# Optimization experiments

Measured on AMD Instinct MI355X. Metric: run time of the kernel, lower is better.

Reference implementation:

```python
import math
import jax, jax.numpy as jnp
import numpy as np

B, N, E, H, DPOS = 64, 196, 768, 16, 3
DH = E // H


def rel_pos(num_patches):
    # deterministic relative-position encodings [N, N, 3] = (dx, dy, d^2)
    v = int(math.isqrt(num_patches))
    ind = jnp.arange(v)[None, :] - jnp.arange(v)[:, None]          # [v, v]
    indx = jnp.tile(ind, (v, v))                                    # [N, N]
    indy = jnp.repeat(jnp.repeat(ind, v, axis=0), v, axis=1)       # [N, N]
    indd = indx ** 2 + indy ** 2
    return jnp.stack([indx, indy, indd], axis=-1).astype(jnp.float32)


def setup_inputs() -> dict:
    key = jax.random.key(0)
    ks = jax.random.split(key, 9)
    std = 0.02  # trunc_normal std used by the module's init
    return {
        "q": jax.random.normal(ks[0], (B, N, E), jnp.float32),
        "k": jax.random.normal(ks[1], (B, N, E), jnp.float32),
        "v": jax.random.normal(ks[2], (B, N, E), jnp.float32),
        "mask": jnp.ones((B, 1, N, N), jnp.bool_),
        "Wq": jax.random.normal(ks[3], (E, E), jnp.float32) * std,
        "Wk": jax.random.normal(ks[4], (E, E), jnp.float32) * std,
        "Wv": jax.random.normal(ks[5], (E, E), jnp.float32) * std,
        "Wo": jax.random.normal(ks[6], (E, E), jnp.float32) * std,
        "bo": jnp.zeros((E,), jnp.float32),
        "Wpos": jax.random.normal(ks[7], (H, DPOS), jnp.float32) * std,
        "bpos": jnp.zeros((H,), jnp.float32),
        "gating": jnp.ones((H,), jnp.float32),
    }


def reference(q, k, v, mask, Wq, Wk, Wv, Wo, bo, Wpos, bpos, gating):
    b, n, _ = q.shape

    def heads(x, W):  # [b, n, E] -> [b, H, n, DH]
        return (x @ W.T).reshape(b, n, H, DH).transpose(0, 2, 1, 3)

    Q, K, V = heads(q, Wq), heads(k, Wk), heads(v, Wv)

    energy = jnp.einsum('bhqd,bhkd->bhqk', Q, K) / math.sqrt(DH)
    energy = jnp.where(mask, energy, -jnp.inf)
    content = jax.nn.softmax(energy, axis=-1)                      # [b, H, n, n]

    rel = rel_pos(n)                                               # [n, n, 3]
    pos = jnp.einsum('qkp,hp->hqk', rel, Wpos) + bpos[:, None, None]
    pos = jax.nn.softmax(pos, axis=-1)[None]                       # [1, H, n, n]

    g = jax.nn.sigmoid(gating)[None, :, None, None]
    score = (1.0 - g) * content + g * pos
    score = score / jnp.sum(score, axis=-1, keepdims=True)

    attn = jnp.einsum('bhqk,bhkd->bhqd', score, V)
    out = attn.transpose(0, 2, 1, 3).reshape(b, n, E) @ Wo.T + bo
    return out
```

## Files before the change

kernel.cpp:

```cpp
#include <hip/hip_runtime.h>
#include <hip/hip_bf16.h>

#define BB 64
#define NN 196
#define EE 768
#define HH 16
#define DHH 48

typedef short bf16x8 __attribute__((ext_vector_type(8)));
typedef float f32x4 __attribute__((ext_vector_type(4)));
typedef unsigned short u16;
typedef unsigned short u16x8 __attribute__((ext_vector_type(8)));
typedef unsigned int u32;

static __device__ __forceinline__ u16 f2bf(float f) {
  union { float f; u32 u; } un; un.f = f;
  u32 u = un.u;
  u32 r = (u + 0x7fffu + ((u >> 16) & 1u)) >> 16;
  return (u16)r;
}

static __device__ __forceinline__ u16 f2bf_hw(float f) {
  __hip_bfloat16 h = __float2bfloat16(f);
  return __builtin_bit_cast(u16, h);
}

#define GLOAD16(GP, LP)                                                        \
  __builtin_amdgcn_global_load_lds(                                            \
      (const __attribute__((address_space(1))) void*)(GP),                     \
      (__attribute__((address_space(3))) void*)(LP), 16, 0, 0)

static __device__ __forceinline__ int xcd_swz(int bid, int nwg) {
  int q = nwg >> 3, r = nwg & 7;
  int xcd = bid & 7, i = bid >> 3;
  return (xcd < r ? xcd * (q + 1) : r * (q + 1) + (xcd - r) * q) + i;
}

__global__ __launch_bounds__(64) void pos_kernel(const float* __restrict__ Wpos,
                                                 const float* __restrict__ bpos,
                                                 float* __restrict__ pos) {
  int bid = blockIdx.x;
  int h = bid / NN, q = bid % NN;
  int lane = threadIdx.x;
  float w0 = Wpos[h * 3 + 0], w1 = Wpos[h * 3 + 1], w2 = Wpos[h * 3 + 2];
  float bb = bpos[h];
  int qx = q % 14, qy = q / 14;
  float e[4];
  float mx = -1e30f;
#pragma unroll
  for (int i = 0; i < 4; ++i) {
    int k = lane + 64 * i;
    float val = -1e30f;
    if (k < NN) {
      int kx = k % 14, ky = k / 14;
      float dx = (float)(kx - qx), dy = (float)(ky - qy);
      val = w0 * dx + w1 * dy + w2 * (dx * dx + dy * dy) + bb;
    }
    e[i] = val;
    mx = fmaxf(mx, val);
  }
#pragma unroll
  for (int off = 1; off < 64; off <<= 1) mx = fmaxf(mx, __shfl_xor(mx, off));
  float s = 0.f;
#pragma unroll
  for (int i = 0; i < 4; ++i) {
    int k = lane + 64 * i;
    float p = (k < NN) ? expf(e[i] - mx) : 0.f;
    e[i] = p;
    s += p;
  }
#pragma unroll
  for (int off = 1; off < 64; off <<= 1) s += __shfl_xor(s, off);
  float inv = 1.f / s;
#pragma unroll
  for (int i = 0; i < 4; ++i) {
    int k = lane + 64 * i;
    if (k < NN) pos[(size_t)h * NN * NN + (size_t)q * NN + k] = e[i] * inv;
  }
}

__global__ __launch_bounds__(256) void cvtw_kernel(const float* __restrict__ W0,
                                                   const float* __restrict__ W1,
                                                   const float* __restrict__ W2,
                                                   const float* __restrict__ W3,
                                                   u16* __restrict__ out) {
  const float* Ws[4] = {W0, W1, W2, W3};
  int mat = blockIdx.y;
  const float* src = Ws[mat];
  int idx = blockIdx.x * 256 + threadIdx.x;
  float4 f = ((const float4*)src)[idx];
  short4 s;
  s.x = (short)f2bf_hw(f.x);
  s.y = (short)f2bf_hw(f.y);
  s.z = (short)f2bf_hw(f.z);
  s.w = (short)f2bf_hw(f.w);
  *(short4*)(out + (size_t)mat * EE * EE + (size_t)idx * 4) = s;
}

template <bool A_BF16, bool OUT_F32>
static __device__ __forceinline__ void gemm_body(const void* __restrict__ Aptr,
                                                 const u16* __restrict__ Wb,
                                                 void* __restrict__ Yptr,
                                                 const float* __restrict__ bias,
                                                 int m0, int n0) {
  __shared__ u16 As[128 * 32];
  __shared__ u16 Bs[128 * 32];
  const int tid = threadIdx.x;
  const int lane = tid & 63, wid = tid >> 6;
  const int wm = wid >> 1, wn = wid & 1;
  const int r16 = lane & 15, g4 = lane >> 4;
  f32x4 acc[4][4];
#pragma unroll
  for (int i = 0; i < 4; ++i)
#pragma unroll
    for (int j = 0; j < 4; ++j) acc[i][j] = (f32x4){0.f, 0.f, 0.f, 0.f};

  const int srow = tid >> 2, sseg = tid & 3;
  const u16* Bg = Wb + (size_t)(n0 + srow) * EE + sseg * 8;

  for (int k0 = 0; k0 < EE; k0 += 32) {
    GLOAD16(Bg + k0, &Bs[tid * 8]);
    GLOAD16(Bg + 64 * EE + k0, &Bs[(256 + tid) * 8]);
    if (A_BF16) {
      const u16* Ag = (const u16*)Aptr + (size_t)(m0 + srow) * EE + sseg * 8 + k0;
      GLOAD16(Ag, &As[tid * 8]);
      GLOAD16(Ag + 64 * EE, &As[(256 + tid) * 8]);
    } else {
#pragma unroll
      for (int c = 0; c < 2; ++c) {
        int idx = c * 256 + tid;
        const float* Ag =
            (const float*)Aptr + (size_t)(m0 + (idx >> 2)) * EE + k0 + (idx & 3) * 8;
        float4 f0 = ((const float4*)Ag)[0];
        float4 f1 = ((const float4*)Ag)[1];
        u16x8 s0;
        s0[0] = f2bf_hw(f0.x); s0[1] = f2bf_hw(f0.y);
        s0[2] = f2bf_hw(f0.z); s0[3] = f2bf_hw(f0.w);
        s0[4] = f2bf_hw(f1.x); s0[5] = f2bf_hw(f1.y);
        s0[6] = f2bf_hw(f1.z); s0[7] = f2bf_hw(f1.w);
        *(u16x8*)&As[idx * 8] = s0;
      }
    }
    __syncthreads();
    bf16x8 af[4], bfr[4];
#pragma unroll
    for (int i = 0; i < 4; ++i)
      af[i] = *(const bf16x8*)&As[(wm * 64 + i * 16 + r16) * 32 + g4 * 8];
#pragma unroll
    for (int j = 0; j < 4; ++j)
      bfr[j] = *(const bf16x8*)&Bs[(wn * 64 + j * 16 + r16) * 32 + g4 * 8];
#pragma unroll
    for (int i = 0; i < 4; ++i)
#pragma unroll
      for (int j = 0; j < 4; ++j)
        acc[i][j] = __builtin_amdgcn_mfma_f32_16x16x32_bf16(af[i], bfr[j], acc[i][j], 0, 0, 0);
    __syncthreads();
  }
#pragma unroll
  for (int i = 0; i < 4; ++i) {
    int row = m0 + wm * 64 + i * 16 + g4 * 4;
#pragma unroll
    for (int j = 0; j < 4; ++j) {
      int col = n0 + wn * 64 + j * 16 + r16;
#pragma unroll
      for (int v = 0; v < 4; ++v) {
        float val = acc[i][j][v];
        if (OUT_F32)
          ((float*)Yptr)[(size_t)(row + v) * EE + col] = val + bias[col];
        else
          ((u16*)Yptr)[(size_t)(row + v) * EE + col] = f2bf(val);
      }
    }
  }
}

__global__ __launch_bounds__(256) void qkv_gemm(const float* __restrict__ q,
                                                const float* __restrict__ k,
                                                const float* __restrict__ v,
                                                const u16* __restrict__ Wqb,
                                                const u16* __restrict__ Wkb,
                                                const u16* __restrict__ Wvb,
                                                u16* __restrict__ Qp,
                                                u16* __restrict__ Kp,
                                                u16* __restrict__ Vp) {
  int sid = xcd_swz(blockIdx.x, 3 * 98 * 6);
  int z = sid / 588, rem = sid % 588;
  int m0 = (rem / 6) * 128, n0 = (rem % 6) * 128;
  const float* A = (z == 0) ? q : (z == 1) ? k : v;
  const u16* W = (z == 0) ? Wqb : (z == 1) ? Wkb : Wvb;
  u16* Y = (z == 0) ? Qp : (z == 1) ? Kp : Vp;
  gemm_body<false, false>(A, W, Y, nullptr, m0, n0);
}

__global__ __launch_bounds__(256) void out_gemm(const u16* __restrict__ ctx,
                                                const u16* __restrict__ Wob,
                                                float* __restrict__ out,
                                                const float* __restrict__ bo) {
  int sid = xcd_swz(blockIdx.x, 98 * 6);
  int m0 = (sid / 6) * 128, n0 = (sid % 6) * 128;
  gemm_body<true, true>(ctx, Wob, out, bo, m0, n0);
}

__global__ __launch_bounds__(512) void attn_kernel(const u16* __restrict__ Qp,
                                                   const u16* __restrict__ Kp,
                                                   const u16* __restrict__ Vp,
                                                   const float* __restrict__ pos,
                                                   const float* __restrict__ gating,
                                                   u16* __restrict__ ctx) {
  __shared__ u16 Qs[208 * 72];
  __shared__ u16 Ks[208 * 72];
  __shared__ u16 Vt[48 * 232];
  __shared__ u16 sc[8][16 * 232];
  int bh = blockIdx.x;
  int b = bh >> 4, h = bh & 15;
  int tid = threadIdx.x;
  {
    u32* z = (u32*)&Qs[0];
    for (int i = tid; i < (208 * 72) / 2; i += 512) z[i] = 0u;
    z = (u32*)&Ks[0];
    for (int i = tid; i < (208 * 72) / 2; i += 512) z[i] = 0u;
    z = (u32*)&Vt[0];
    for (int i = tid; i < (48 * 232) / 2; i += 512) z[i] = 0u;
  }
  __syncthreads();
  const u16* Qb = Qp + (size_t)b * NN * EE + h * DHH;
  const u16* Kb = Kp + (size_t)b * NN * EE + h * DHH;
  const u16* Vb = Vp + (size_t)b * NN * EE + h * DHH;
  for (int c = tid; c < NN * 12; c += 512) {
    int row = c / 12, k4 = (c % 12) * 4;
    short4 v = *(const short4*)(Qb + (size_t)row * EE + k4);
    *(short4*)&Qs[row * 72 + k4] = v;
  }
  for (int c = tid; c < NN * 12; c += 512) {
    int row = c / 12, k4 = (c % 12) * 4;
    short4 v = *(const short4*)(Kb + (size_t)row * EE + k4);
    *(short4*)&Ks[row * 72 + k4] = v;
  }
  for (int c = tid; c < NN * 12; c += 512) {
    int key = c / 12, d4 = (c % 12) * 4;
    short4 v = *(const short4*)(Vb + (size_t)key * EE + d4);
    Vt[(d4 + 0) * 232 + key] = (u16)v.x;
    Vt[(d4 + 1) * 232 + key] = (u16)v.y;
    Vt[(d4 + 2) * 232 + key] = (u16)v.z;
    Vt[(d4 + 3) * 232 + key] = (u16)v.w;
  }
  __syncthreads();

  int wid = tid >> 6, lane = tid & 63;
  int r16 = lane & 15, g4 = lane >> 4;
  float g = 1.f / (1.f + expf(-gating[h]));
  float omg = 1.f - g;
  u16* scw = &sc[wid][0];
  const float scale = 0.14433756729740643f;
  const float* posh = pos + (size_t)h * NN * NN;

  for (int rt = wid; rt < 13; rt += 8) {
    int q0 = rt * 16;
    bf16x8 aQ0 = *(const bf16x8*)&Qs[(q0 + r16) * 72 + g4 * 8];
    bf16x8 aQ1 = *(const bf16x8*)&Qs[(q0 + r16) * 72 + 32 + g4 * 8];
    f32x4 e[13];
#pragma unroll
    for (int ct = 0; ct < 13; ++ct) {
      bf16x8 b0 = *(const bf16x8*)&Ks[(ct * 16 + r16) * 72 + g4 * 8];
      bf16x8 b1 = *(const bf16x8*)&Ks[(ct * 16 + r16) * 72 + 32 + g4 * 8];
      f32x4 t = (f32x4){0.f, 0.f, 0.f, 0.f};
      t = __builtin_amdgcn_mfma_f32_16x16x32_bf16(aQ0, b0, t, 0, 0, 0);
      t = __builtin_amdgcn_mfma_f32_16x16x32_bf16(aQ1, b1, t, 0, 0, 0);
      e[ct] = t;
    }
    float mx[4] = {-1e30f, -1e30f, -1e30f, -1e30f};
#pragma unroll
    for (int ct = 0; ct < 13; ++ct) {
      int cix = ct * 16 + r16;
      bool valid = cix < NN;
#pragma unroll
      for (int v = 0; v < 4; ++v) {
        float ev = e[ct][v] * scale;
        ev = valid ? ev : -1e30f;
        e[ct][v] = ev;
        mx[v] = fmaxf(mx[v], ev);
      }
    }
#pragma unroll
    for (int v = 0; v < 4; ++v)
#pragma unroll
      for (int off = 1; off < 16; off <<= 1) mx[v] = fmaxf(mx[v], __shfl_xor(mx[v], off));
    float sm[4] = {0.f, 0.f, 0.f, 0.f};
#pragma unroll
    for (int ct = 0; ct < 13; ++ct)
#pragma unroll
      for (int v = 0; v < 4; ++v) {
        float p = __expf(e[ct][v] - mx[v]);
        e[ct][v] = p;
        sm[v] += p;
      }
#pragma unroll
    for (int v = 0; v < 4; ++v)
#pragma unroll
      for (int off = 1; off < 16; off <<= 1) sm[v] += __shfl_xor(sm[v], off);
    float inv[4];
#pragma unroll
    for (int v = 0; v < 4; ++v) inv[v] = 1.f / sm[v];
    int qg[4];
#pragma unroll
    for (int v = 0; v < 4; ++v) qg[v] = q0 + g4 * 4 + v;
    float t2[4] = {0.f, 0.f, 0.f, 0.f};
#pragma unroll
    for (int ct = 0; ct < 13; ++ct) {
      int cix = ct * 16 + r16;
      bool valid = cix < NN;
#pragma unroll
      for (int v = 0; v < 4; ++v) {
        float content = e[ct][v] * inv[v];
        float pv = 0.f;
        if (valid && qg[v] < NN) pv = posh[(size_t)qg[v] * NN + cix];
        float s = omg * content + g * pv;
        e[ct][v] = s;
        t2[v] += s;
      }
    }
#pragma unroll
    for (int v = 0; v < 4; ++v)
#pragma unroll
      for (int off = 1; off < 16; off <<= 1) t2[v] += __shfl_xor(t2[v], off);
    float inv2[4];
#pragma unroll
    for (int v = 0; v < 4; ++v) inv2[v] = 1.f / t2[v];
#pragma unroll
    for (int ct = 0; ct < 14; ++ct)
#pragma unroll
      for (int v = 0; v < 4; ++v) {
        float s = (ct < 13) ? e[ct][v] * inv2[v] : 0.f;
        scw[(g4 * 4 + v) * 232 + ct * 16 + r16] = f2bf(s);
      }
    asm volatile("s_waitcnt lgkmcnt(0)" ::: "memory");
#pragma unroll
    for (int dt = 0; dt < 3; ++dt) {
      f32x4 pv = (f32x4){0.f, 0.f, 0.f, 0.f};
#pragma unroll
      for (int kt = 0; kt < 7; ++kt) {
        bf16x8 aS = *(const bf16x8*)&scw[r16 * 232 + kt * 32 + g4 * 8];
        bf16x8 bV = *(const bf16x8*)&Vt[(dt * 16 + r16) * 232 + kt * 32 + g4 * 8];
        pv = __builtin_amdgcn_mfma_f32_16x16x32_bf16(aS, bV, pv, 0, 0, 0);
      }
#pragma unroll
      for (int v = 0; v < 4; ++v) {
        if (qg[v] < NN)
          ctx[((size_t)b * NN + qg[v]) * EE + h * DHH + dt * 16 + r16] = f2bf(pv[v]);
      }
    }
  }
}

extern "C" void kernel_launch(void* const* d_in, const int* in_sizes, int n_in,
                              void* d_out, int out_size, void* d_ws, size_t ws_size,
                              hipStream_t stream) {
  const float* q = (const float*)d_in[0];
  const float* k = (const float*)d_in[1];
  const float* v = (const float*)d_in[2];
  const float* Wq = (const float*)d_in[4];
  const float* Wk = (const float*)d_in[5];
  const float* Wv = (const float*)d_in[6];
  const float* Wo = (const float*)d_in[7];
  const float* bo = (const float*)d_in[8];
  const float* Wpos = (const float*)d_in[9];
  const float* bpos = (const float*)d_in[10];
  const float* gating = (const float*)d_in[11];
  float* out = (float*)d_out;

  char* ws = (char*)d_ws;
  const size_t elems = (size_t)BB * NN * EE;
  u16* Qp = (u16*)ws;
  u16* Kp = Qp + elems;
  u16* Vp = Kp + elems;
  u16* ctx = Vp + elems;
  float* pos = (float*)(ws + 4 * elems * sizeof(u16));
  u16* Wqb = (u16*)(ws + 4 * elems * sizeof(u16) + (size_t)HH * NN * NN * sizeof(float));
  u16* Wkb = Wqb + (size_t)EE * EE;
  u16* Wvb = Wkb + (size_t)EE * EE;
  u16* Wob = Wvb + (size_t)EE * EE;

  hipLaunchKernelGGL(pos_kernel, dim3(HH * NN), dim3(64), 0, stream, Wpos, bpos, pos);
  hipLaunchKernelGGL(cvtw_kernel, dim3(EE * EE / 4 / 256, 4), dim3(256), 0, stream,
                     Wq, Wk, Wv, Wo, Wqb);

  hipLaunchKernelGGL(qkv_gemm, dim3(3 * 98 * 6), dim3(256), 0, stream,
                     q, k, v, Wqb, Wkb, Wvb, Qp, Kp, Vp);

  hipLaunchKernelGGL(attn_kernel, dim3(BB * HH), dim3(512), 0, stream,
                     Qp, Kp, Vp, pos, gating, ctx);

  hipLaunchKernelGGL(out_gemm, dim3(98 * 6), dim3(256), 0, stream,
                     ctx, Wob, out, bo);
}
```

Measured before the change: 199.8 us.

## Double-buffer GEMM LDS tiles and load fp32 A directly via async copies

Restructures the shared GEMM body into a two-stage pipeline: the next K-slice of A and B is issued with direct global-to-LDS loads while MFMAs run on the current buffer, removing one barrier per iteration. For the fp32-input QKV projection, A is no longer converted through registers before the LDS store. It is copied raw as fp32 into LDS with an XOR swizzle and converted to bf16 when fragments are read. This trades double the LDS footprint (fp32 A tile plus two buffers) and extra conversion work per fragment read for latency hiding and fewer register round-trips.

```diff
diff --git a/kernel.cpp b/kernel.cpp
--- a/kernel.cpp
+++ b/kernel.cpp
@@ -97,14 +97,15 @@
   *(short4*)(out + (size_t)mat * EE * EE + (size_t)idx * 4) = s;
 }
 
-template <bool A_BF16, bool OUT_F32>
+template <bool A_F32, bool OUT_F32>
 static __device__ __forceinline__ void gemm_body(const void* __restrict__ Aptr,
                                                  const u16* __restrict__ Wb,
                                                  void* __restrict__ Yptr,
                                                  const float* __restrict__ bias,
                                                  int m0, int n0) {
-  __shared__ u16 As[128 * 32];
-  __shared__ u16 Bs[128 * 32];
+  constexpr int ABYTES = A_F32 ? (128 * 32 * 4) : (128 * 32 * 2);
+  __shared__ unsigned char Asb[2][ABYTES];
+  __shared__ u16 Bs[2][128 * 32];
   const int tid = threadIdx.x;
   const int lane = tid & 63, wid = tid >> 6;
   const int wm = wid >> 1, wn = wid & 1;
@@ -115,46 +116,66 @@
 #pragma unroll
     for (int j = 0; j < 4; ++j) acc[i][j] = (f32x4){0.f, 0.f, 0.f, 0.f};
 
-  const int srow = tid >> 2, sseg = tid & 3;
-  const u16* Bg = Wb + (size_t)(n0 + srow) * EE + sseg * 8;
-
-  for (int k0 = 0; k0 < EE; k0 += 32) {
-    GLOAD16(Bg + k0, &Bs[tid * 8]);
-    GLOAD16(Bg + 64 * EE + k0, &Bs[(256 + tid) * 8]);
-    if (A_BF16) {
-      const u16* Ag = (const u16*)Aptr + (size_t)(m0 + srow) * EE + sseg * 8 + k0;
-      GLOAD16(Ag, &As[tid * 8]);
-      GLOAD16(Ag + 64 * EE, &As[(256 + tid) * 8]);
+  auto stage = [&](int buf, int k0) {
+#pragma unroll
+    for (int c = 0; c < 2; ++c) {
+      int s = c * 256 + tid;
+      GLOAD16(Wb + (size_t)(n0 + (s >> 2)) * EE + k0 + (s & 3) * 8,
+              (u16*)&Bs[buf][0] + s * 8);
+    }
+    if (A_F32) {
+#pragma unroll
+      for (int c = 0; c < 4; ++c) {
+        int s = c * 256 + tid;
+        int row = s >> 3;
+        int cf = ((s & 7) ^ (row & 7)) * 4;
+        GLOAD16((const float*)Aptr + (size_t)(m0 + row) * EE + k0 + cf,
+                &Asb[buf][0] + s * 16);
+      }
     } else {
 #pragma unroll
       for (int c = 0; c < 2; ++c) {
-        int idx = c * 256 + tid;
-        const float* Ag =
-            (const float*)Aptr + (size_t)(m0 + (idx >> 2)) * EE + k0 + (idx & 3) * 8;
-        float4 f0 = ((const float4*)Ag)[0];
-        float4 f1 = ((const float4*)Ag)[1];
-        u16x8 s0;
-        s0[0] = f2bf_hw(f0.x); s0[1] = f2bf_hw(f0.y);
-        s0[2] = f2bf_hw(f0.z); s0[3] = f2bf_hw(f0.w);
-        s0[4] = f2bf_hw(f1.x); s0[5] = f2bf_hw(f1.y);
-        s0[6] = f2bf_hw(f1.z); s0[7] = f2bf_hw(f1.w);
-        *(u16x8*)&As[idx * 8] = s0;
-      }
-    }
-    __syncthreads();
+        int s = c * 256 + tid;
+        GLOAD16((const u16*)Aptr + (size_t)(m0 + (s >> 2)) * EE + k0 + (s & 3) * 8,
+                &Asb[buf][0] + s * 16);
+      }
+    }
+  };
+
+  stage(0, 0);
+  __syncthreads();
+  int buf = 0;
+  for (int t = 0; t < 24; ++t) {
+    if (t < 23) stage(buf ^ 1, (t + 1) * 32);
     bf16x8 af[4], bfr[4];
 #pragma unroll
-    for (int i = 0; i < 4; ++i)
-      af[i] = *(const bf16x8*)&As[(wm * 64 + i * 16 + r16) * 32 + g4 * 8];
+    for (int i = 0; i < 4; ++i) {
+      int r = wm * 64 + i * 16 + r16;
+      if (A_F32) {
+        const char* rowp = (const char*)&Asb[buf][0] + r * 128;
+        int lo = (g4 * 32) ^ ((r & 7) << 4);
+        f32x4 l4 = *(const f32x4*)(rowp + lo);
+        f32x4 h4 = *(const f32x4*)(rowp + (lo ^ 16));
+        u16x8 fr;
+        fr[0] = f2bf_hw(l4[0]); fr[1] = f2bf_hw(l4[1]);
+        fr[2] = f2bf_hw(l4[2]); fr[3] = f2bf_hw(l4[3]);
+        fr[4] = f2bf_hw(h4[0]); fr[5] = f2bf_hw(h4[1]);
+        fr[6] = f2bf_hw(h4[2]); fr[7] = f2bf_hw(h4[3]);
+        af[i] = __builtin_bit_cast(bf16x8, fr);
+      } else {
+        af[i] = *(const bf16x8*)((const u16*)&Asb[buf][0] + r * 32 + g4 * 8);
+      }
+    }
 #pragma unroll
     for (int j = 0; j < 4; ++j)
-      bfr[j] = *(const bf16x8*)&Bs[(wn * 64 + j * 16 + r16) * 32 + g4 * 8];
+      bfr[j] = *(const bf16x8*)&Bs[buf][(wn * 64 + j * 16 + r16) * 32 + g4 * 8];
 #pragma unroll
     for (int i = 0; i < 4; ++i)
 #pragma unroll
       for (int j = 0; j < 4; ++j)
         acc[i][j] = __builtin_amdgcn_mfma_f32_16x16x32_bf16(af[i], bfr[j], acc[i][j], 0, 0, 0);
     __syncthreads();
+    buf ^= 1;
   }
 #pragma unroll
   for (int i = 0; i < 4; ++i) {
@@ -189,7 +210,7 @@
   const float* A = (z == 0) ? q : (z == 1) ? k : v;
   const u16* W = (z == 0) ? Wqb : (z == 1) ? Wkb : Wvb;
   u16* Y = (z == 0) ? Qp : (z == 1) ? Kp : Vp;
-  gemm_body<false, false>(A, W, Y, nullptr, m0, n0);
+  gemm_body<true, false>(A, W, Y, nullptr, m0, n0);
 }
 
 __global__ __launch_bounds__(256) void out_gemm(const u16* __restrict__ ctx,
@@ -198,7 +219,7 @@
                                                 const float* __restrict__ bo) {
   int sid = xcd_swz(blockIdx.x, 98 * 6);
   int m0 = (sid / 6) * 128, n0 = (sid % 6) * 128;
-  gemm_body<true, true>(ctx, Wob, out, bo, m0, n0);
+  gemm_body<false, true>(ctx, Wob, out, bo, m0, n0);
 }
 
 __global__ __launch_bounds__(512) void attn_kernel(const u16* __restrict__ Qp,
```

New measurement: 200.5 us. About the same (+0.4%).

## Triple-buffer GEMM tiles with 512-thread 128x256 blocks and async prefetch

Applied to the files above, without the earlier changes.

The shared GEMM body switches to 128x256 output tiles computed by 8 waves and keeps a three-stage LDS ring buffer. Loads for step t+2 are issued while the MFMAs for step t run, and explicit waitcnt plus barrier replace the two syncthreads per k-step. For fp32 A inputs the global loads are held in registers and converted to bf16 after the MFMAs, to hide load latency behind compute. MFMA priority is raised with s_setprio. The LDS footprint grows and fewer blocks are launched, which may hurt occupancy or wave balance on the device.

```diff
diff --git a/kernel.cpp b/kernel.cpp
--- a/kernel.cpp
+++ b/kernel.cpp
@@ -97,17 +97,17 @@
   *(short4*)(out + (size_t)mat * EE * EE + (size_t)idx * 4) = s;
 }
 
-template <bool A_BF16, bool OUT_F32>
+template <bool A_F32, bool OUT_F32>
 static __device__ __forceinline__ void gemm_body(const void* __restrict__ Aptr,
                                                  const u16* __restrict__ Wb,
                                                  void* __restrict__ Yptr,
                                                  const float* __restrict__ bias,
                                                  int m0, int n0) {
-  __shared__ u16 As[128 * 32];
-  __shared__ u16 Bs[128 * 32];
+  __shared__ u16 As[3][128 * 32];
+  __shared__ u16 Bs[3][256 * 32];
   const int tid = threadIdx.x;
   const int lane = tid & 63, wid = tid >> 6;
-  const int wm = wid >> 1, wn = wid & 1;
+  const int wm = wid >> 2, wn = wid & 3;
   const int r16 = lane & 15, g4 = lane >> 4;
   f32x4 acc[4][4];
 #pragma unroll
@@ -115,47 +115,84 @@
 #pragma unroll
     for (int j = 0; j < 4; ++j) acc[i][j] = (f32x4){0.f, 0.f, 0.f, 0.f};
 
-  const int srow = tid >> 2, sseg = tid & 3;
-  const u16* Bg = Wb + (size_t)(n0 + srow) * EE + sseg * 8;
-
-  for (int k0 = 0; k0 < EE; k0 += 32) {
-    GLOAD16(Bg + k0, &Bs[tid * 8]);
-    GLOAD16(Bg + 64 * EE + k0, &Bs[(256 + tid) * 8]);
-    if (A_BF16) {
-      const u16* Ag = (const u16*)Aptr + (size_t)(m0 + srow) * EE + sseg * 8 + k0;
-      GLOAD16(Ag, &As[tid * 8]);
-      GLOAD16(Ag + 64 * EE, &As[(256 + tid) * 8]);
+  const int arow = tid >> 2, aq = tid & 3;
+  float4 fa0, fa1;
+
+  auto loadA = [&](int k0) {
+    const float* p = (const float*)Aptr + (size_t)(m0 + arow) * EE + k0 + aq * 8;
+    fa0 = ((const float4*)p)[0];
+    fa1 = ((const float4*)p)[1];
+  };
+  auto writeA = [&](int b) {
+    u16x8 s;
+    s[0] = f2bf_hw(fa0.x); s[1] = f2bf_hw(fa0.y);
+    s[2] = f2bf_hw(fa0.z); s[3] = f2bf_hw(fa0.w);
+    s[4] = f2bf_hw(fa1.x); s[5] = f2bf_hw(fa1.y);
+    s[6] = f2bf_hw(fa1.z); s[7] = f2bf_hw(fa1.w);
+    *(u16x8*)&As[b][arow * 32 + aq * 8] = s;
+  };
+  auto gloadA = [&](int b, int k0) {
+    GLOAD16((const u16*)Aptr + (size_t)(m0 + arow) * EE + k0 + aq * 8,
+            &As[b][tid * 8]);
+  };
+  auto gloadB = [&](int b, int k0) {
+#pragma unroll
+    for (int c = 0; c < 2; ++c) {
+      int s = c * 512 + tid;
+      GLOAD16(Wb + (size_t)(n0 + (s >> 2)) * EE + k0 + (s & 3) * 8,
+              &Bs[b][s * 8]);
+    }
+  };
+
+  if constexpr (A_F32) {
+    loadA(0);  gloadB(0, 0);  writeA(0);
+    loadA(32); gloadB(1, 32); writeA(1);
+  } else {
+    gloadA(0, 0);  gloadB(0, 0);
+    gloadA(1, 32); gloadB(1, 32);
+  }
+  asm volatile("s_waitcnt lgkmcnt(0)" ::: "memory");
+  asm volatile("s_waitcnt vmcnt(2)" ::: "memory");
+  asm volatile("s_barrier" ::: "memory");
+
+  for (int t = 0; t < 24; ++t) {
+    const int cb = t % 3;
+    const int sb = (t + 2) % 3;
+    const bool st = (t + 2) < 24;
+    if (st) {
+      if constexpr (A_F32) loadA((t + 2) * 32);
+      else                 gloadA(sb, (t + 2) * 32);
+      gloadB(sb, (t + 2) * 32);
+    }
+    bf16x8 af[4], bf[4];
+#pragma unroll
+    for (int i = 0; i < 4; ++i)
+      af[i] = *(const bf16x8*)&As[cb][(wm * 64 + i * 16 + r16) * 32 + g4 * 8];
+#pragma unroll
+    for (int j = 0; j < 4; ++j)
+      bf[j] = *(const bf16x8*)&Bs[cb][(wn * 64 + j * 16 + r16) * 32 + g4 * 8];
+    __builtin_amdgcn_s_setprio(1);
+#pragma unroll
+    for (int i = 0; i < 4; ++i)
+#pragma unroll
+      for (int j = 0; j < 4; ++j)
+        acc[i][j] = __builtin_amdgcn_mfma_f32_16x16x32_bf16(af[i], bf[j], acc[i][j], 0, 0, 0);
+    __builtin_amdgcn_s_setprio(0);
+    if (st) {
+      if constexpr (A_F32) writeA(sb);
+    }
+    asm volatile("s_waitcnt lgkmcnt(0)" ::: "memory");
+    if (t < 22) {
+      if constexpr (A_F32)
+        asm volatile("s_waitcnt vmcnt(2)" ::: "memory");
+      else
+        asm volatile("s_waitcnt vmcnt(3)" ::: "memory");
     } else {
-#pragma unroll
-      for (int c = 0; c < 2; ++c) {
-        int idx = c * 256 + tid;
-        const float* Ag =
-            (const float*)Aptr + (size_t)(m0 + (idx >> 2)) * EE + k0 + (idx & 3) * 8;
-        float4 f0 = ((const float4*)Ag)[0];
-        float4 f1 = ((const float4*)Ag)[1];
-        u16x8 s0;
-        s0[0] = f2bf_hw(f0.x); s0[1] = f2bf_hw(f0.y);
-        s0[2] = f2bf_hw(f0.z); s0[3] = f2bf_hw(f0.w);
-        s0[4] = f2bf_hw(f1.x); s0[5] = f2bf_hw(f1.y);
-        s0[6] = f2bf_hw(f1.z); s0[7] = f2bf_hw(f1.w);
-        *(u16x8*)&As[idx * 8] = s0;
-      }
-    }
-    __syncthreads();
-    bf16x8 af[4], bfr[4];
-#pragma unroll
-    for (int i = 0; i < 4; ++i)
-      af[i] = *(const bf16x8*)&As[(wm * 64 + i * 16 + r16) * 32 + g4 * 8];
-#pragma unroll
-    for (int j = 0; j < 4; ++j)
-      bfr[j] = *(const bf16x8*)&Bs[(wn * 64 + j * 16 + r16) * 32 + g4 * 8];
-#pragma unroll
-    for (int i = 0; i < 4; ++i)
-#pragma unroll
-      for (int j = 0; j < 4; ++j)
-        acc[i][j] = __builtin_amdgcn_mfma_f32_16x16x32_bf16(af[i], bfr[j], acc[i][j], 0, 0, 0);
-    __syncthreads();
-  }
+      asm volatile("s_waitcnt vmcnt(0)" ::: "memory");
+    }
+    asm volatile("s_barrier" ::: "memory");
+  }
+
 #pragma unroll
   for (int i = 0; i < 4; ++i) {
     int row = m0 + wm * 64 + i * 16 + g4 * 4;
@@ -174,31 +211,31 @@
   }
 }
 
-__global__ __launch_bounds__(256) void qkv_gemm(const float* __restrict__ q,
-                                                const float* __restrict__ k,
-                                                const float* __restrict__ v,
-                                                const u16* __restrict__ Wqb,
-                                                const u16* __restrict__ Wkb,
-                                                const u16* __restrict__ Wvb,
-                                                u16* __restrict__ Qp,
-                                                u16* __restrict__ Kp,
-                                                u16* __restrict__ Vp) {
-  int sid = xcd_swz(blockIdx.x, 3 * 98 * 6);
-  int z = sid / 588, rem = sid % 588;
-  int m0 = (rem / 6) * 128, n0 = (rem % 6) * 128;
+__global__ __launch_bounds__(512, 4) void qkv_gemm(const float* __restrict__ q,
+                                                   const float* __restrict__ k,
+                                                   const float* __restrict__ v,
+                                                   const u16* __restrict__ Wqb,
+                                                   const u16* __restrict__ Wkb,
+                                                   const u16* __restrict__ Wvb,
+                                                   u16* __restrict__ Qp,
+                                                   u16* __restrict__ Kp,
+                                                   u16* __restrict__ Vp) {
+  int sid = xcd_swz(blockIdx.x, 3 * 98 * 3);
+  int z = sid / 294, rem = sid % 294;
+  int m0 = (rem / 3) * 128, n0 = (rem % 3) * 256;
   const float* A = (z == 0) ? q : (z == 1) ? k : v;
   const u16* W = (z == 0) ? Wqb : (z == 1) ? Wkb : Wvb;
   u16* Y = (z == 0) ? Qp : (z == 1) ? Kp : Vp;
-  gemm_body<false, false>(A, W, Y, nullptr, m0, n0);
-}
-
-__global__ __launch_bounds__(256) void out_gemm(const u16* __restrict__ ctx,
-                                                const u16* __restrict__ Wob,
-                                                float* __restrict__ out,
-                                                const float* __restrict__ bo) {
-  int sid = xcd_swz(blockIdx.x, 98 * 6);
-  int m0 = (sid / 6) * 128, n0 = (sid % 6) * 128;
-  gemm_body<true, true>(ctx, Wob, out, bo, m0, n0);
+  gemm_body<true, false>(A, W, Y, nullptr, m0, n0);
+}
+
+__global__ __launch_bounds__(512, 4) void out_gemm(const u16* __restrict__ ctx,
+                                                   const u16* __restrict__ Wob,
+                                                   float* __restrict__ out,
+                                                   const float* __restrict__ bo) {
+  int sid = xcd_swz(blockIdx.x, 98 * 3);
+  int m0 = (sid / 3) * 128, n0 = (sid % 3) * 256;
+  gemm_body<false, true>(ctx, Wob, out, bo, m0, n0);
 }
 
 __global__ __launch_bounds__(512) void attn_kernel(const u16* __restrict__ Qp,
@@ -384,12 +421,12 @@
   hipLaunchKernelGGL(cvtw_kernel, dim3(EE * EE / 4 / 256, 4), dim3(256), 0, stream,
                      Wq, Wk, Wv, Wo, Wqb);
 
-  hipLaunchKernelGGL(qkv_gemm, dim3(3 * 98 * 6), dim3(256), 0, stream,
+  hipLaunchKernelGGL(qkv_gemm, dim3(3 * 98 * 3), dim3(512), 0, stream,
                      q, k, v, Wqb, Wkb, Wvb, Qp, Kp, Vp);
 
   hipLaunchKernelGGL(attn_kernel, dim3(BB * HH), dim3(512), 0, stream,
                      Qp, Kp, Vp, pos, gating, ctx);
 
-  hipLaunchKernelGGL(out_gemm, dim3(98 * 6), dim3(256), 0, stream,
+  hipLaunchKernelGGL(out_gemm, dim3(98 * 3), dim3(512), 0, stream,
                      ctx, Wob, out, bo);
 }
```

After: 192.2 us. 1.04x faster.
